# Kernel optimization log

Measured on AMD Instinct MI355X. Metric: run time of the kernel, lower is better.

The kernel has to match this reference:

```python
import jax, jax.numpy as jnp
import numpy as np

N = 100000        # nodes
E = 3200000       # random edges (avg degree 32); self-loops added in reference
IN, HID, HEADS, OUT = 10, 32, 2, 4
NEG_SLOPE = 0.2   # PyG GATConv default leaky_relu slope


def setup_inputs() -> dict:
    key = jax.random.key(0)
    ks = jax.random.split(key, 16)
    s = 0.1
    return {
        "x": jax.random.normal(ks[0], (N, IN), jnp.float32),
        "edge_index": jax.random.randint(ks[1], (2, E), 0, N),
        "W1": jax.random.normal(ks[2], (IN, HEADS * HID), jnp.float32) * s,
        "a1s": jax.random.normal(ks[3], (HEADS, HID), jnp.float32) * s,
        "a1d": jax.random.normal(ks[4], (HEADS, HID), jnp.float32) * s,
        "b1": jnp.zeros((HEADS * HID,), jnp.float32),
        "W2": jax.random.normal(ks[5], (HEADS * HID, HEADS * HID), jnp.float32) * s,
        "a2s": jax.random.normal(ks[6], (HEADS, HID), jnp.float32) * s,
        "a2d": jax.random.normal(ks[7], (HEADS, HID), jnp.float32) * s,
        "b2": jnp.zeros((HEADS * HID,), jnp.float32),
        "W3": jax.random.normal(ks[8], (HEADS * HID, OUT), jnp.float32) * s,
        "a3s": jax.random.normal(ks[9], (1, OUT), jnp.float32) * s,
        "a3d": jax.random.normal(ks[10], (1, OUT), jnp.float32) * s,
        "b3": jnp.zeros((OUT,), jnp.float32),
    }


def gat_layer(x, src, dst, W, a_src, a_dst, b, concat):
    """One PyG-style GATConv (shared src/dst linear, self-loops already in src/dst)."""
    heads, oc = a_src.shape
    h = (x @ W).reshape(-1, heads, oc)                    # [N, H, C]
    asc = jnp.einsum('nhc,hc->nh', h, a_src)              # [N, H]
    adc = jnp.einsum('nhc,hc->nh', h, a_dst)              # [N, H]
    e = jax.nn.leaky_relu(asc[src] + adc[dst], NEG_SLOPE) # [Etot, H]
    m = jax.ops.segment_max(e, dst, num_segments=N)       # segment softmax over dst
    ex = jnp.exp(e - m[dst])
    z = jax.ops.segment_sum(ex, dst, num_segments=N)
    alpha = ex / z[dst]                                   # [Etot, H]
    out = jax.ops.segment_sum(h[src] * alpha[:, :, None], dst, num_segments=N)
    out = out.reshape(-1, heads * oc) if concat else out.mean(axis=1)
    return out + b


def reference(x, edge_index, W1, a1s, a1d, b1, W2, a2s, a2d, b2, W3, a3s, a3d, b3):
    loops = jnp.arange(N)
    src = jnp.concatenate([edge_index[0], loops])
    dst = jnp.concatenate([edge_index[1], loops])
    h = jax.nn.relu(gat_layer(x, src, dst, W1, a1s, a1d, b1, True))
    h = jax.nn.relu(gat_layer(h, src, dst, W2, a2s, a2d, b2, True))
    h = gat_layer(h, src, dst, W3, a3s, a3d, b3, False)
    return jax.nn.sigmoid(h) * 100.0
```

## Files before the change

### kernel.cpp

```cpp
#include <hip/hip_runtime.h>
#include <hip/hip_bf16.h>
#include <math.h>

#define NEG_SLOPE 0.2f
#define PSHIFT 8
#define PSIZE 256
#define NPARTS_MAX 392
#define B1 768
#define CELL_CAP 32
#define PCAP 10240
#define LCSR_CAP 10240

typedef int vint2 __attribute__((ext_vector_type(2)));
typedef int vint4 __attribute__((ext_vector_type(4)));
typedef short bf16x8 __attribute__((ext_vector_type(8)));
typedef float floatx4 __attribute__((ext_vector_type(4)));

__device__ __forceinline__ float lrelu(float v) { return fmaxf(v, NEG_SLOPE * v); }

__device__ __forceinline__ unsigned short f2bf(float f) {
    unsigned int b = __float_as_uint(f);
    b += 0x7fffu + ((b >> 16) & 1u);
    return (unsigned short)(b >> 16);
}
__device__ __forceinline__ float bf2f(unsigned short u) {
    return __uint_as_float((unsigned int)u << 16);
}

__global__ void k_part(const int* __restrict__ src, const int* __restrict__ dst, int E,
                       int* __restrict__ pairs, int* __restrict__ ptot, int nparts) {
    __shared__ int stage[NPARTS_MAX * CELL_CAP];
    __shared__ int lcnt[NPARTS_MAX];
    int tid = threadIdx.x, blk = blockIdx.x;
    for (int i = tid; i < nparts; i += 256) lcnt[i] = 0;
    __syncthreads();
    int per = ((E + B1 * 4 - 1) / (B1 * 4)) * 4;
    int s = blk * per, e = min(E, s + per);
    bool al = ((E & 3) == 0);
    for (int i0 = s + tid * 4; i0 < e; i0 += 1024) {
        int dv[4], sv[4], nv;
        if (al && i0 + 4 <= e) {
            vint4 d4 = __builtin_nontemporal_load((const vint4*)(dst + i0));
            vint4 s4 = __builtin_nontemporal_load((const vint4*)(src + i0));
            dv[0] = d4.x; dv[1] = d4.y; dv[2] = d4.z; dv[3] = d4.w;
            sv[0] = s4.x; sv[1] = s4.y; sv[2] = s4.z; sv[3] = s4.w;
            nv = 4;
        } else {
            nv = min(4, e - i0);
            for (int k = 0; k < nv; ++k) {
                dv[k] = __builtin_nontemporal_load(dst + i0 + k);
                sv[k] = __builtin_nontemporal_load(src + i0 + k);
            }
        }
        for (int k = 0; k < nv; ++k) {
            int p = dv[k] >> PSHIFT;
            int pos = atomicAdd(&lcnt[p], 1);
            if (pos < CELL_CAP)
                stage[p * CELL_CAP + pos] = (sv[k] << PSHIFT) | (dv[k] & (PSIZE - 1));
        }
    }
    __syncthreads();
    for (int p = tid; p < nparts; p += 256) {
        int tgt = min(lcnt[p], CELL_CAP);
        if (tgt == 0) continue;
        int base = atomicAdd(&ptot[p], tgt);
        if (base + tgt > PCAP) tgt = max(0, PCAP - base);
        int* gp = pairs + (size_t)p * PCAP + base;
        const int* sp = &stage[p * CELL_CAP];
        for (int j = 0; j < tgt; ++j) gp[j] = sp[j];
    }
}

__global__ void k_pscan(const int* __restrict__ ptot, int* __restrict__ pbase,
                        int* __restrict__ row, int nparts, int N) {
    __shared__ int sh[512];
    int tid = threadIdx.x;
    int v = (tid < nparts) ? min(ptot[tid], PCAP) : 0;
    sh[tid] = v;
    __syncthreads();
    for (int off = 1; off < 512; off <<= 1) {
        int t = (tid >= off) ? sh[tid - off] : 0;
        __syncthreads();
        sh[tid] += t;
        __syncthreads();
    }
    if (tid < nparts) pbase[tid] = sh[tid] - v;
    if (tid == nparts - 1) row[N] = sh[tid];
}

__global__ void k_scat2(const int* __restrict__ pairs, const int* __restrict__ ptot,
                        const int* __restrict__ pbase, int* __restrict__ row,
                        int* __restrict__ csr, int N) {
    __shared__ int lcsr[LCSR_CAP];
    __shared__ int lhist[PSIZE], lcur[PSIZE];
    int part = blockIdx.x;
    int lo = part << PSHIFT;
    int npart = min(PSIZE, N - lo);
    int tid = threadIdx.x;
    int cnt = min(ptot[part], PCAP);
    const int* seg = pairs + (size_t)part * PCAP;
    for (int i = tid; i < PSIZE; i += 1024) lhist[i] = 0;
    __syncthreads();
    for (int i = tid; i < cnt; i += 1024)
        atomicAdd(&lhist[__builtin_nontemporal_load(&seg[i]) & (PSIZE - 1)], 1);
    __syncthreads();
    if (tid < PSIZE) lcur[tid] = lhist[tid];
    __syncthreads();
    for (int off = 1; off < PSIZE; off <<= 1) {
        int t = 0;
        if (tid < PSIZE && tid >= off) t = lcur[tid - off];
        __syncthreads();
        if (tid < PSIZE) lcur[tid] += t;
        __syncthreads();
    }
    int pb = pbase[part];
    if (tid < npart) row[lo + tid] = pb + lcur[tid] - lhist[tid];
    if (tid < PSIZE) lcur[tid] -= lhist[tid];
    __syncthreads();
    for (int i = tid; i < cnt; i += 1024) {
        int v = __builtin_nontemporal_load(&seg[i]);
        int pos = atomicAdd(&lcur[v & (PSIZE - 1)], 1);
        if (pos < LCSR_CAP) lcsr[pos] = (unsigned)v >> PSHIFT;
    }
    __syncthreads();
    for (int i = tid; i < cnt; i += 1024)
        csr[pb + i] = lcsr[i];
}

__global__ void k_lin1(const float* __restrict__ x, const float* __restrict__ W,
                       const float* __restrict__ as_, const float* __restrict__ ad_,
                       unsigned short* __restrict__ hb, float* __restrict__ asc,
                       float* __restrict__ adc, int N) {
    __shared__ float sW[10 * 64];
    int tid = threadIdx.x;
    for (int i = tid; i < 640; i += 256) sW[i] = W[i];
    __syncthreads();
    int wid = tid >> 6, lane = tid & 63;
    int n = blockIdx.x * 4 + wid;
    if (n >= N) return;
    float acc = 0.f;
#pragma unroll
    for (int k = 0; k < 10; ++k) acc += x[n * 10 + k] * sW[k * 64 + lane];
    hb[(size_t)n * 64 + lane] = f2bf(acc);
    int head = lane >> 5, cc = lane & 31;
    float rs = acc * as_[lane];
    float rd = acc * ad_[lane];
#pragma unroll
    for (int m = 16; m >= 1; m >>= 1) {
        rs += __shfl_xor(rs, m, 64);
        rd += __shfl_xor(rd, m, 64);
    }
    if (cc == 0) { asc[n * 2 + head] = rs; adc[n * 2 + head] = rd; }
}

__global__ void k_lin2(const float* __restrict__ yin, const float* __restrict__ W,
                       const float* __restrict__ as_, const float* __restrict__ ad_,
                       unsigned short* __restrict__ hb, float* __restrict__ asc,
                       float* __restrict__ adc, int N) {
    __shared__ unsigned short sW[64 * 64];
    int tid = threadIdx.x;
    for (int i = tid; i < 4096; i += 256) sW[i] = f2bf(W[i]);
    __syncthreads();
    int wid = tid >> 6, lane = tid & 63;
    int quad = lane >> 4, col = lane & 15;
    bf16x8 bfr[4][2];
#pragma unroll
    for (int blk = 0; blk < 4; ++blk)
#pragma unroll
        for (int kh = 0; kh < 2; ++kh)
#pragma unroll
            for (int j = 0; j < 8; ++j)
                bfr[blk][kh][j] = (short)sW[(kh * 32 + quad * 8 + j) * 64 + blk * 16 + col];
    float asv[4], adv[4];
#pragma unroll
    for (int blk = 0; blk < 4; ++blk) {
        asv[blk] = as_[blk * 16 + col];
        adv[blk] = ad_[blk * 16 + col];
    }
    int tile = blockIdx.x * 4 + wid;
    int nb = tile * 16;
    if (nb >= N) return;
    int mrow = nb + col; if (mrow >= N) mrow = N - 1;
    const float* yr = yin + (size_t)mrow * 64;
    bf16x8 afr[2];
#pragma unroll
    for (int kh = 0; kh < 2; ++kh) {
        const float4* p = (const float4*)(yr + kh * 32 + quad * 8);
        float4 u0 = p[0], u1 = p[1];
        afr[kh][0] = (short)f2bf(u0.x); afr[kh][1] = (short)f2bf(u0.y);
        afr[kh][2] = (short)f2bf(u0.z); afr[kh][3] = (short)f2bf(u0.w);
        afr[kh][4] = (short)f2bf(u1.x); afr[kh][5] = (short)f2bf(u1.y);
        afr[kh][6] = (short)f2bf(u1.z); afr[kh][7] = (short)f2bf(u1.w);
    }
    floatx4 acc[4];
#pragma unroll
    for (int blk = 0; blk < 4; ++blk) {
        acc[blk][0] = 0.f; acc[blk][1] = 0.f; acc[blk][2] = 0.f; acc[blk][3] = 0.f;
        acc[blk] = __builtin_amdgcn_mfma_f32_16x16x32_bf16(afr[0], bfr[blk][0], acc[blk], 0, 0, 0);
        acc[blk] = __builtin_amdgcn_mfma_f32_16x16x32_bf16(afr[1], bfr[blk][1], acc[blk], 0, 0, 0);
    }
#pragma unroll
    for (int r = 0; r < 4; ++r) {
        int m = nb + quad * 4 + r;
        if (m < N) {
#pragma unroll
            for (int blk = 0; blk < 4; ++blk)
                hb[(size_t)m * 64 + blk * 16 + col] = f2bf(acc[blk][r]);
        }
    }
    float s0[4], s1[4], d0[4], d1[4];
#pragma unroll
    for (int r = 0; r < 4; ++r) {
        s0[r] = acc[0][r] * asv[0] + acc[1][r] * asv[1];
        s1[r] = acc[2][r] * asv[2] + acc[3][r] * asv[3];
        d0[r] = acc[0][r] * adv[0] + acc[1][r] * adv[1];
        d1[r] = acc[2][r] * adv[2] + acc[3][r] * adv[3];
    }
#pragma unroll
    for (int mask = 8; mask >= 1; mask >>= 1) {
#pragma unroll
        for (int r = 0; r < 4; ++r) {
            s0[r] += __shfl_xor(s0[r], mask, 64);
            s1[r] += __shfl_xor(s1[r], mask, 64);
            d0[r] += __shfl_xor(d0[r], mask, 64);
            d1[r] += __shfl_xor(d1[r], mask, 64);
        }
    }
    if (col < 4) {
        int m = nb + quad * 4 + col;
        if (m < N) {
            float vs0 = col == 0 ? s0[0] : col == 1 ? s0[1] : col == 2 ? s0[2] : s0[3];
            float vs1 = col == 0 ? s1[0] : col == 1 ? s1[1] : col == 2 ? s1[2] : s1[3];
            float vd0 = col == 0 ? d0[0] : col == 1 ? d0[1] : col == 2 ? d0[2] : d0[3];
            float vd1 = col == 0 ? d1[0] : col == 1 ? d1[1] : col == 2 ? d1[2] : d1[3];
            asc[m * 2 + 0] = vs0; asc[m * 2 + 1] = vs1;
            adc[m * 2 + 0] = vd0; adc[m * 2 + 1] = vd1;
        }
    }
}

__global__ void k_agg(const unsigned short* __restrict__ hb, const float* __restrict__ asc,
                      const float* __restrict__ adc, const int* __restrict__ row,
                      const int* __restrict__ csr_src, const float* __restrict__ bias,
                      float* __restrict__ yout, int N, int do_relu) {
    __shared__ vint2 tbl[4][64];
    int tid = threadIdx.x;
    int wid = tid >> 6, lane = tid & 63;
    int n = blockIdx.x * 4 + wid;
    if (n >= N) return;
    int s = row[n], e = row[n + 1];
    int head = lane >> 5, sub = lane & 31;
    int chq = lane & 15;
    int hq = chq >> 3;
    int jo = lane >> 4;
    float2 ad = ((const float2*)adc)[n];
    float adch = head ? ad.y : ad.x;
    float2 asf = ((const float2*)asc)[n];
    float p_self_h = __expf(lrelu((head ? asf.y : asf.x) + adch));
    float zl = (sub == 0) ? p_self_h : 0.f;
    float a0 = 0.f, a1 = 0.f, a2 = 0.f, a3 = 0.f;
    const vint2* hb64 = (const vint2*)hb;
    for (int base = s; base < e; base += 32) {
        int cnt = e - base; if (cnt > 32) cnt = 32;
        int idx = base + sub;
        int srcv = 0;
        float p_l = 0.f;
        if (idx < e) {
            srcv = csr_src[idx];
            p_l = __expf(lrelu(asc[(size_t)srcv * 2 + head] + adch));
        }
        zl += p_l;
        vint2 ent; ent.x = srcv; ent.y = __float_as_int(p_l);
        tbl[wid][(head << 5) | sub] = ent;
        __builtin_amdgcn_wave_barrier();
        int tb = hq << 5;
#pragma unroll 2
        for (int j = jo; j < cnt; j += 4) {
            vint2 t = tbl[wid][tb | j];
            vint2 pk = hb64[(size_t)t.x * 16 + chq];
            float p = __int_as_float(t.y);
            unsigned int pa = (unsigned int)pk.x, pb = (unsigned int)pk.y;
            a0 += p * __uint_as_float(pa << 16);
            a1 += p * __uint_as_float(pa & 0xffff0000u);
            a2 += p * __uint_as_float(pb << 16);
            a3 += p * __uint_as_float(pb & 0xffff0000u);
        }
        __builtin_amdgcn_wave_barrier();
    }
    a0 += __shfl_xor(a0, 16, 64); a1 += __shfl_xor(a1, 16, 64);
    a2 += __shfl_xor(a2, 16, 64); a3 += __shfl_xor(a3, 16, 64);
    a0 += __shfl_xor(a0, 32, 64); a1 += __shfl_xor(a1, 32, 64);
    a2 += __shfl_xor(a2, 32, 64); a3 += __shfl_xor(a3, 32, 64);
#pragma unroll
    for (int msk = 16; msk >= 1; msk >>= 1) zl += __shfl_xor(zl, msk, 64);
    float zo = __shfl_xor(zl, 32, 64);
    float zneed = (hq == head) ? zl : zo;
    float adcm = hq ? ad.y : ad.x;
    float p_self_my = __expf(lrelu((hq ? asf.y : asf.x) + adcm));
    vint2 pks = hb64[(size_t)n * 16 + chq];
    unsigned int sa = (unsigned int)pks.x, sb = (unsigned int)pks.y;
    a0 += p_self_my * __uint_as_float(sa << 16);
    a1 += p_self_my * __uint_as_float(sa & 0xffff0000u);
    a2 += p_self_my * __uint_as_float(sb << 16);
    a3 += p_self_my * __uint_as_float(sb & 0xffff0000u);
    float inv = 1.f / zneed;
    float4 bv = ((const float4*)bias)[chq];
    float y0 = a0 * inv + bv.x;
    float y1 = a1 * inv + bv.y;
    float y2 = a2 * inv + bv.z;
    float y3 = a3 * inv + bv.w;
    if (do_relu) {
        y0 = fmaxf(y0, 0.f); y1 = fmaxf(y1, 0.f);
        y2 = fmaxf(y2, 0.f); y3 = fmaxf(y3, 0.f);
    }
    if (lane < 16) {
        float4 o; o.x = y0; o.y = y1; o.z = y2; o.w = y3;
        ((float4*)yout)[(size_t)n * 16 + chq] = o;
    }
}

__global__ void k_lin3(const float* __restrict__ yin, const float* __restrict__ W3,
                       const float* __restrict__ a3s, const float* __restrict__ a3d,
                       float* __restrict__ h3, float* __restrict__ asc3, float* __restrict__ adc3,
                       int N) {
    __shared__ float sW[256];
    int tid = threadIdx.x;
    sW[tid] = W3[tid];
    __syncthreads();
    int t = blockIdx.x * 256 + tid;
    int n = t >> 2, c = t & 3;
    if (n >= N) return;
    float acc = 0.f;
#pragma unroll
    for (int k = 0; k < 64; ++k) acc += yin[(size_t)n * 64 + k] * sW[k * 4 + c];
    h3[(size_t)n * 4 + c] = acc;
    float rs = acc * a3s[c], rd = acc * a3d[c];
    rs += __shfl_xor(rs, 1, 64); rs += __shfl_xor(rs, 2, 64);
    rd += __shfl_xor(rd, 1, 64); rd += __shfl_xor(rd, 2, 64);
    if (c == 0) { asc3[n] = rs; adc3[n] = rd; }
}

__global__ void k_agg3(const float* __restrict__ h3, const float* __restrict__ asc3,
                       const float* __restrict__ adc3, const int* __restrict__ row,
                       const int* __restrict__ csr_src, const float* __restrict__ b3,
                       float* __restrict__ out, int N) {
    int tid = threadIdx.x;
    int wid = tid >> 6, lane = tid & 63;
    int n = blockIdx.x * 4 + wid;
    if (n >= N) return;
    int s = row[n], e = row[n + 1];
    float adcn = adc3[n];
    float p_self = __expf(lrelu(asc3[n] + adcn));
    int c = lane & 3, jg = lane >> 2;
    float num = (jg == 0) ? p_self * h3[(size_t)n * 4 + c] : 0.f;
    float den = (jg == 0) ? p_self : 0.f;
    for (int base = s; base < e; base += 16) {
        int idx = base + jg;
        if (idx < e) {
            int src = csr_src[idx];
            float p = __expf(lrelu(asc3[src] + adcn));
            num += p * h3[(size_t)src * 4 + c];
            den += p;
        }
    }
#pragma unroll
    for (int mask = 4; mask <= 32; mask <<= 1) {
        num += __shfl_xor(num, mask, 64);
        den += __shfl_xor(den, mask, 64);
    }
    if (lane < 4) {
        float v = num / den + b3[c];
        out[n * 4 + c] = 100.f / (1.f + __expf(-v));
    }
}

extern "C" void kernel_launch(void* const* d_in, const int* in_sizes, int n_in,
                              void* d_out, int out_size, void* d_ws, size_t ws_size,
                              hipStream_t stream) {
    const float* x   = (const float*)d_in[0];
    const int*   ei  = (const int*)d_in[1];
    const float* W1  = (const float*)d_in[2];
    const float* a1s = (const float*)d_in[3];
    const float* a1d = (const float*)d_in[4];
    const float* b1  = (const float*)d_in[5];
    const float* W2  = (const float*)d_in[6];
    const float* a2s = (const float*)d_in[7];
    const float* a2d = (const float*)d_in[8];
    const float* b2  = (const float*)d_in[9];
    const float* W3  = (const float*)d_in[10];
    const float* a3s = (const float*)d_in[11];
    const float* a3d = (const float*)d_in[12];
    const float* b3  = (const float*)d_in[13];
    float* out = (float*)d_out;

    const int N = in_sizes[0] / 10;
    const int E = in_sizes[1] / 2;
    const int* esrc = ei;
    const int* edst = ei + E;
    const int nparts = (N + PSIZE - 1) >> PSHIFT;

    char* ws = (char*)d_ws;
    size_t off = 0;
    auto alloc = [&](size_t bytes) {
        void* p = ws + off;
        off = (off + bytes + 255) & ~(size_t)255;
        return p;
    };
    int*   row   = (int*)alloc((size_t)(N + 1) * sizeof(int));
    int*   ptot  = (int*)alloc(NPARTS_MAX * sizeof(int));
    int*   pbase = (int*)alloc(NPARTS_MAX * sizeof(int));
    int*   csr   = (int*)alloc((size_t)E * sizeof(int));
    unsigned short* hb = (unsigned short*)alloc((size_t)N * 64 * sizeof(unsigned short));
    float* y     = (float*)alloc((size_t)N * 64 * sizeof(float));
    float* l3scr = (float*)alloc((size_t)N * 6 * sizeof(float));
    float* asc   = (float*)alloc((size_t)N * 2 * sizeof(float));
    float* adc   = (float*)alloc((size_t)N * 2 * sizeof(float));
    float* h3   = l3scr;
    float* asc3 = l3scr + (size_t)N * 4;
    float* adc3 = l3scr + (size_t)N * 5;
    int* pairs = (int*)hb;

    (void)hipMemsetAsync(ptot, 0, NPARTS_MAX * sizeof(int), stream);

    const int nw = (N + 3) / 4;
    const int tiles = (N + 15) / 16;

    k_part<<<B1, 256, 0, stream>>>(esrc, edst, E, pairs, ptot, nparts);
    k_pscan<<<1, 512, 0, stream>>>(ptot, pbase, row, nparts, N);
    k_scat2<<<nparts, 1024, 0, stream>>>(pairs, ptot, pbase, row, csr, N);

    k_lin1<<<nw, 256, 0, stream>>>(x, W1, a1s, a1d, hb, asc, adc, N);
    k_agg<<<nw, 256, 0, stream>>>(hb, asc, adc, row, csr, b1, y, N, 1);
    k_lin2<<<(tiles + 3) / 4, 256, 0, stream>>>(y, W2, a2s, a2d, hb, asc, adc, N);
    k_agg<<<nw, 256, 0, stream>>>(hb, asc, adc, row, csr, b2, y, N, 1);
    k_lin3<<<(N * 4 + 255) / 256, 256, 0, stream>>>(y, W3, a3s, a3d, h3, asc3, adc3, N);
    k_agg3<<<nw, 256, 0, stream>>>(h3, asc3, adc3, row, csr, b3, out, N);
}
```

Measured before the change: 373.4 us.

## Pack layer-3 features and logits into one 16-byte record per node

Layer 3 now writes a single 16-byte record per node: the four output features packed as bf16 plus the source and destination attention logits. The final aggregation gathers one record per edge instead of separate h3 and asc3 loads. Each lane now handles whole edges with a 64-way stride rather than splitting channels across lanes. The aggregation loop for the first two layers is also unrolled 4 instead of 2. Storing h3 in bf16 reduces precision in the last layer's outputs.

Result: faster. 358.5 us (-4.0%).

```diff
diff --git a/kernel.cpp b/kernel.cpp
--- a/kernel.cpp
+++ b/kernel.cpp
@@ -274,7 +274,7 @@
         tbl[wid][(head << 5) | sub] = ent;
         __builtin_amdgcn_wave_barrier();
         int tb = hq << 5;
-#pragma unroll 2
+#pragma unroll 4
         for (int j = jo; j < cnt; j += 4) {
             vint2 t = tbl[wid][tb | j];
             vint2 pk = hb64[(size_t)t.x * 16 + chq];
@@ -321,8 +321,7 @@
 
 __global__ void k_lin3(const float* __restrict__ yin, const float* __restrict__ W3,
                        const float* __restrict__ a3s, const float* __restrict__ a3d,
-                       float* __restrict__ h3, float* __restrict__ asc3, float* __restrict__ adc3,
-                       int N) {
+                       float4* __restrict__ rec, int N) {
     __shared__ float sW[256];
     int tid = threadIdx.x;
     sW[tid] = W3[tid];
@@ -333,15 +332,23 @@
     float acc = 0.f;
 #pragma unroll
     for (int k = 0; k < 64; ++k) acc += yin[(size_t)n * 64 + k] * sW[k * 4 + c];
-    h3[(size_t)n * 4 + c] = acc;
     float rs = acc * a3s[c], rd = acc * a3d[c];
     rs += __shfl_xor(rs, 1, 64); rs += __shfl_xor(rs, 2, 64);
     rd += __shfl_xor(rd, 1, 64); rd += __shfl_xor(rd, 2, 64);
-    if (c == 0) { asc3[n] = rs; adc3[n] = rd; }
-}
-
-__global__ void k_agg3(const float* __restrict__ h3, const float* __restrict__ asc3,
-                       const float* __restrict__ adc3, const int* __restrict__ row,
+    float a_1 = __shfl_xor(acc, 1, 64);
+    float a_2 = __shfl_xor(acc, 2, 64);
+    float a_3 = __shfl_xor(acc, 3, 64);
+    if (c == 0) {
+        unsigned int lo = (unsigned int)f2bf(acc) | ((unsigned int)f2bf(a_1) << 16);
+        unsigned int hi = (unsigned int)f2bf(a_2) | ((unsigned int)f2bf(a_3) << 16);
+        float4 r;
+        r.x = __uint_as_float(lo); r.y = __uint_as_float(hi);
+        r.z = rs; r.w = rd;
+        rec[n] = r;
+    }
+}
+
+__global__ void k_agg3(const float4* __restrict__ rec, const int* __restrict__ row,
                        const int* __restrict__ csr_src, const float* __restrict__ b3,
                        float* __restrict__ out, int N) {
     int tid = threadIdx.x;
@@ -349,28 +356,41 @@
     int n = blockIdx.x * 4 + wid;
     if (n >= N) return;
     int s = row[n], e = row[n + 1];
-    float adcn = adc3[n];
-    float p_self = __expf(lrelu(asc3[n] + adcn));
-    int c = lane & 3, jg = lane >> 2;
-    float num = (jg == 0) ? p_self * h3[(size_t)n * 4 + c] : 0.f;
-    float den = (jg == 0) ? p_self : 0.f;
-    for (int base = s; base < e; base += 16) {
-        int idx = base + jg;
-        if (idx < e) {
-            int src = csr_src[idx];
-            float p = __expf(lrelu(asc3[src] + adcn));
-            num += p * h3[(size_t)src * 4 + c];
-            den += p;
-        }
-    }
-#pragma unroll
-    for (int mask = 4; mask <= 32; mask <<= 1) {
-        num += __shfl_xor(num, mask, 64);
-        den += __shfl_xor(den, mask, 64);
+    float4 rn = rec[n];
+    float adcn = rn.w;
+    float n0 = 0.f, n1 = 0.f, n2 = 0.f, n3 = 0.f, den = 0.f;
+    if (lane == 0) {
+        float p = __expf(lrelu(rn.z + adcn));
+        unsigned int lo = __float_as_uint(rn.x), hi = __float_as_uint(rn.y);
+        n0 = p * __uint_as_float(lo << 16);
+        n1 = p * __uint_as_float(lo & 0xffff0000u);
+        n2 = p * __uint_as_float(hi << 16);
+        n3 = p * __uint_as_float(hi & 0xffff0000u);
+        den = p;
+    }
+    for (int idx = s + lane; idx < e; idx += 64) {
+        int src = csr_src[idx];
+        float4 r = rec[src];
+        float p = __expf(lrelu(r.z + adcn));
+        unsigned int lo = __float_as_uint(r.x), hi = __float_as_uint(r.y);
+        n0 += p * __uint_as_float(lo << 16);
+        n1 += p * __uint_as_float(lo & 0xffff0000u);
+        n2 += p * __uint_as_float(hi << 16);
+        n3 += p * __uint_as_float(hi & 0xffff0000u);
+        den += p;
+    }
+#pragma unroll
+    for (int msk = 32; msk >= 1; msk >>= 1) {
+        n0 += __shfl_xor(n0, msk, 64);
+        n1 += __shfl_xor(n1, msk, 64);
+        n2 += __shfl_xor(n2, msk, 64);
+        n3 += __shfl_xor(n3, msk, 64);
+        den += __shfl_xor(den, msk, 64);
     }
     if (lane < 4) {
-        float v = num / den + b3[c];
-        out[n * 4 + c] = 100.f / (1.f + __expf(-v));
+        float num = lane == 0 ? n0 : lane == 1 ? n1 : lane == 2 ? n2 : n3;
+        float v = num / den + b3[lane];
+        out[n * 4 + lane] = 100.f / (1.f + __expf(-v));
     }
 }
 
@@ -412,12 +432,9 @@
     int*   csr   = (int*)alloc((size_t)E * sizeof(int));
     unsigned short* hb = (unsigned short*)alloc((size_t)N * 64 * sizeof(unsigned short));
     float* y     = (float*)alloc((size_t)N * 64 * sizeof(float));
-    float* l3scr = (float*)alloc((size_t)N * 6 * sizeof(float));
+    float4* rec  = (float4*)alloc((size_t)N * sizeof(float4));
     float* asc   = (float*)alloc((size_t)N * 2 * sizeof(float));
     float* adc   = (float*)alloc((size_t)N * 2 * sizeof(float));
-    float* h3   = l3scr;
-    float* asc3 = l3scr + (size_t)N * 4;
-    float* adc3 = l3scr + (size_t)N * 5;
     int* pairs = (int*)hb;
 
     (void)hipMemsetAsync(ptot, 0, NPARTS_MAX * sizeof(int), stream);
@@ -433,6 +450,6 @@
     k_agg<<<nw, 256, 0, stream>>>(hb, asc, adc, row, csr, b1, y, N, 1);
     k_lin2<<<(tiles + 3) / 4, 256, 0, stream>>>(y, W2, a2s, a2d, hb, asc, adc, N);
     k_agg<<<nw, 256, 0, stream>>>(hb, asc, adc, row, csr, b2, y, N, 1);
-    k_lin3<<<(N * 4 + 255) / 256, 256, 0, stream>>>(y, W3, a3s, a3d, h3, asc3, adc3, N);
-    k_agg3<<<nw, 256, 0, stream>>>(h3, asc3, adc3, row, csr, b3, out, N);
-}
+    k_lin3<<<(N * 4 + 255) / 256, 256, 0, stream>>>(y, W3, a3s, a3d, rec, N);
+    k_agg3<<<nw, 256, 0, stream>>>(rec, row, csr, b3, out, N);
+}
```
